# Optimization experiments

Hardware: AMD Instinct MI355X
Metric: run time of the kernel (lower is better)

The kernel has to match this reference:

```python
import jax, jax.numpy as jnp
import numpy as np

N = 50_000        # nodes
E = 1_600_000     # edges (avg degree 32)
H = 64            # hidden_channels
DEPTH = 3         # -> 2*DEPTH mid conv layers


def setup_inputs() -> dict:
    key = jax.random.key(0)
    ks = jax.random.split(key, 8)
    x = jax.random.normal(ks[0], (N, 1), dtype=jnp.float32)
    edge_index = jax.random.randint(ks[1], (2, E), 0, N, dtype=jnp.int32)
    s = 0.1  # small init scale
    W_in = s * jax.random.normal(ks[2], (2 * 1 + 1, H), dtype=jnp.float32)
    b_in = jnp.zeros((H,), jnp.float32)
    W_mid = s * jax.random.normal(ks[3], (2 * DEPTH, 2 * H + 1, H), dtype=jnp.float32)
    b_mid = jnp.zeros((2 * DEPTH, H), jnp.float32)
    W_out = s * jax.random.normal(ks[4], (2 * H + 1, 1), dtype=jnp.float32)
    b_out = jnp.zeros((1,), jnp.float32)
    return {"x": x, "edge_index": edge_index, "W_in": W_in, "b_in": b_in,
            "W_mid": W_mid, "b_mid": b_mid, "W_out": W_out, "b_out": b_out}


def _conv(x, src, dst, sign, inv_deg, W, b):
    """Directional_EdgeConv: mean_{j->i} Linear([x_i, x_j - x_i, sign(j-i)])."""
    x_i = x[dst]                                   # [E, F] target feats
    x_j = x[src]                                   # [E, F] source feats
    feat = jnp.concatenate([x_i, x_j - x_i, sign], axis=-1)  # [E, 2F+1]
    msg = feat @ W + b                             # [E, out]
    agg = jax.ops.segment_sum(msg, dst, num_segments=x.shape[0])  # [N, out]
    return agg * inv_deg                           # mean aggregation


def reference(x, edge_index, W_in, b_in, W_mid, b_mid, W_out, b_out):
    src = edge_index[0]
    dst = edge_index[1]
    # vectorized replacement of the per-edge Python sign loop
    sign = jnp.sign((src - dst).astype(x.dtype))[:, None]        # [E, 1]
    deg = jax.ops.segment_sum(jnp.ones((src.shape[0],), x.dtype), dst,
                              num_segments=x.shape[0])
    inv_deg = (1.0 / jnp.maximum(deg, 1.0))[:, None]             # [N, 1]

    x2 = _conv(x, src, dst, sign, inv_deg, W_in, b_in)
    for l in range(DEPTH):
        x1 = jax.nn.leaky_relu(
            _conv(x2, src, dst, sign, inv_deg, W_mid[2 * l], b_mid[2 * l]))
        x2 = jax.nn.leaky_relu(
            _conv(x1, src, dst, sign, inv_deg, W_mid[2 * l + 1], b_mid[2 * l + 1]) + x2)
    return _conv(x2, src, dst, sign, inv_deg, W_out, b_out) + x
```

## Files before the change

kernel.cpp:

```cpp
#include <hip/hip_runtime.h>
#include <hip/hip_fp16.h>

#define HDIM 64
#define NEG_SLOPE 0.01f
#define CAPB 8192
#define BCAP 6144

typedef _Float16 half8 __attribute__((ext_vector_type(8)));
typedef float f32x4 __attribute__((ext_vector_type(4)));

static __device__ __forceinline__ float h_lo(unsigned d) {
    return __half2float(__ushort_as_half((unsigned short)(d & 0xffffu)));
}
static __device__ __forceinline__ float h_hi(unsigned d) {
    return __half2float(__ushort_as_half((unsigned short)(d >> 16)));
}
static __device__ __forceinline__ unsigned packh(float a, float b) {
    unsigned short ra = __half_as_ushort(__float2half(a));
    unsigned short rb = __half_as_ushort(__float2half(b));
    return ((unsigned)rb << 16) | (unsigned)ra;
}
static __device__ __forceinline__ half8 u4h(uint4 v) {
    union { uint4 u; half8 h; } x; x.u = v; return x.h;
}
static __device__ __forceinline__ __half2 uh2(unsigned u) {
    union { unsigned u; __half2 h; } x; x.u = u; return x.h;
}

__global__ void k_setup(int ptotal, const float* __restrict__ W_mid,
                        unsigned short* __restrict__ WTh,
                        int NB, int* gcur, int N, unsigned* xAP, unsigned* xBP,
                        float* tvec) {
    int i = blockIdx.x * blockDim.x + threadIdx.x;
    if (i < ptotal) {
        int l = i >> 13;
        int rem = i & 8191;
        int h = rem >> 7;
        int k = rem & 127;
        const float* W = W_mid + (size_t)l * 129 * 64;
        float v = W[k * 64 + h] - ((k < 64) ? W[(64 + k) * 64 + h] : 0.f);
        WTh[i] = __half_as_ushort(__float2half(v));
    }
    if (i < NB) gcur[i] = i * CAPB;
    if (i < 32) xAP[(size_t)N * 32 + i] = 0u;
    else if (i < 64) xBP[(size_t)N * 32 + (i - 32)] = 0u;
    else if (i == 64) tvec[N] = 0.f;
}

__global__ __launch_bounds__(1024) void k_bucket(
        int E, const int* __restrict__ src, const int* __restrict__ dst,
        int* gcur, unsigned* __restrict__ bucketed, int NB) {
    __shared__ int lh[512];
    __shared__ int lbase[512];
    int t = threadIdx.x;
    int e0 = blockIdx.x * 2048;
    if (t < 512) lh[t] = 0;
    __syncthreads();
    int e1 = e0 + t, e2 = e0 + 1024 + t;
    int d1 = (e1 < E) ? dst[e1] : -1;
    int d2 = (e2 < E) ? dst[e2] : -1;
    if (d1 >= 0) atomicAdd(&lh[((unsigned)d1) >> 7], 1);
    if (d2 >= 0) atomicAdd(&lh[((unsigned)d2) >> 7], 1);
    __syncthreads();
    if (t < NB) {
        int c = lh[t];
        lbase[t] = (c > 0) ? atomicAdd(&gcur[t], c) : 0;
        lh[t] = 0;
    }
    __syncthreads();
    int s1 = (e1 < E) ? src[e1] : 0;
    int s2 = (e2 < E) ? src[e2] : 0;
    if (d1 >= 0) {
        int b = ((unsigned)d1) >> 7;
        int r = atomicAdd(&lh[b], 1);
        int pos = lbase[b] + r;
        if (pos < (b + 1) * CAPB)
            bucketed[pos] = ((unsigned)d1 << 16) | (unsigned)s1;
    }
    if (d2 >= 0) {
        int b = ((unsigned)d2) >> 7;
        int r = atomicAdd(&lh[b], 1);
        int pos = lbase[b] + r;
        if (pos < (b + 1) * CAPB)
            bucketed[pos] = ((unsigned)d2 << 16) | (unsigned)s2;
    }
}

__global__ void k_bktscan(int NB, int N, const int* __restrict__ gcur,
                          int* gstart, int* rowptr) {
    __shared__ int sd[512];
    int t = threadIdx.x;
    int c = (t < NB) ? min(gcur[t] - t * CAPB, CAPB) : 0;
    sd[t] = c;
    __syncthreads();
    int x = c;
    for (int s = 1; s < 512; s <<= 1) {
        int p = (t >= s) ? sd[t - s] : 0;
        __syncthreads();
        x += p;
        sd[t] = x;
        __syncthreads();
    }
    if (t < NB) gstart[t] = x - c;
    if (t == NB - 1) {
        gstart[NB] = x;
        rowptr[N] = x;
    }
}

__global__ void k_csr(int N, const unsigned* __restrict__ bucketed, const int* __restrict__ gcur,
                      const int* __restrict__ gstart, unsigned short* __restrict__ csr,
                      unsigned short* __restrict__ pcsr,
                      int* __restrict__ rowptr, float* __restrict__ ssinv) {
    __shared__ unsigned st[BCAP];
    __shared__ int hist[128], cur[128], excl[128], sgp[128];
    int b = blockIdx.x, t = threadIdx.x;
    int n0 = b << 7;
    int nn = min(128, N - n0);
    int cnt = min(gcur[b] - b * CAPB, CAPB);
    int base = gstart[b];
    if (t < 128) { hist[t] = 0; sgp[t] = 0; }
    unsigned sent = ((unsigned)N << 16) | (unsigned)N;
    unsigned* pb32 = (unsigned*)(pcsr + ((size_t)b << 13));
    for (int i = t; i < 4096; i += 256) pb32[i] = sent;
    __syncthreads();
    bool single = (cnt <= BCAP);
    for (int off = 0; off < cnt; off += BCAP) {
        int bs = min(BCAP, cnt - off);
        for (int i = t; i < bs; i += 256) {
            unsigned w = bucketed[b * CAPB + off + i];
            if (single) st[i] = w;
            int d = (int)(w >> 16);
            int s = (int)(w & 0xffffu);
            int dl = d - n0;
            atomicAdd(&hist[dl], 1);
            atomicAdd(&sgp[dl], ((s < d) ? 1024 : 0) + ((s == d) ? 1 : 0));
        }
    }
    __syncthreads();
    int deg_t = (t < 128) ? hist[t] : 0;
    int x = deg_t;
    for (int s = 1; s < 128; s <<= 1) {
        int p = (t < 128 && t >= s) ? hist[t - s] : 0;
        __syncthreads();
        if (t < 128) { x += p; hist[t] = x; }
        __syncthreads();
    }
    if (t < 128) {
        int ex = hist[t] - deg_t;
        excl[t] = ex;
        cur[t] = ex;
        if (t < nn) {
            rowptr[n0 + t] = base + ex;
            int sg = sgp[t];
            int lt = sg >> 10, eq = sg & 1023;
            float ss = (float)(deg_t - eq - 2 * lt);
            ssinv[n0 + t] = (deg_t > 0) ? ss / (float)deg_t : 0.f;
        }
    }
    __syncthreads();
    for (int off = 0; off < cnt; off += BCAP) {
        int bs = min(BCAP, cnt - off);
        if (!single) {
            for (int i = t; i < bs; i += 256) st[i] = bucketed[b * CAPB + off + i];
            __syncthreads();
        }
        for (int i = t; i < bs; i += 256) {
            unsigned w = st[i];
            int dl = (int)(w >> 16) - n0;
            unsigned short sval = (unsigned short)(w & 0xffffu);
            int p = atomicAdd(&cur[dl], 1);
            csr[base + p] = sval;
            int r = p - excl[dl];
            if (r < 64) pcsr[((size_t)(n0 + dl) << 6) + r] = sval;
        }
        if (!single) __syncthreads();
    }
}

__global__ void k_in(int N, const float* __restrict__ x0,
                     const int* __restrict__ rowptr, const unsigned short* __restrict__ csr,
                     const float* __restrict__ ssinv,
                     const float* __restrict__ W_in, const float* __restrict__ b_in,
                     unsigned* __restrict__ xoutP) {
    int wid = blockIdx.x * (blockDim.x >> 6) + (threadIdx.x >> 6);
    int lane = threadIdx.x & 63;
    if (wid >= N) return;
    int beg = rowptr[wid], end = rowptr[wid + 1];
    int deg = end - beg;
    float s = 0.f;
    for (int e = beg + lane; e < end; e += 64) s += x0[csr[e]];
    for (int m = 32; m >= 1; m >>= 1) s += __shfl_xor(s, m, 64);
    float invd = 1.f / (float)max(deg, 1);
    float mean = s * invd;
    float xi = x0[wid];
    float w1 = W_in[lane], w2 = W_in[64 + lane], w3 = W_in[128 + lane];
    float y = xi * (w1 - w2) + mean * w2 + ssinv[wid] * w3 + b_in[lane];
    if (deg == 0) y = 0.f;
    float ylo = __shfl(y, (2 * lane) & 63, 64);
    float yhi = __shfl(y, (2 * lane + 1) & 63, 64);
    unsigned pkd = packh(ylo, yhi);
    if (lane < 32) xoutP[(size_t)wid * 32 + lane] = pkd;
}

static __device__ __forceinline__ void chunk_acc(
        const uint4* __restrict__ xin16, int sv, int base, int sub, int lq,
        __half2& c0, __half2& c1, __half2& c2, __half2& c3) {
    int s0 = __shfl(sv, base + sub, 64);
    int s1 = __shfl(sv, base + 8 + sub, 64);
    int s2 = __shfl(sv, base + 16 + sub, 64);
    int s3 = __shfl(sv, base + 24 + sub, 64);
    uint4 d0 = xin16[(size_t)s0 * 8 + lq];
    uint4 d1 = xin16[(size_t)s1 * 8 + lq];
    uint4 d2 = xin16[(size_t)s2 * 8 + lq];
    uint4 d3 = xin16[(size_t)s3 * 8 + lq];
    c0 = __hadd2(c0, __hadd2(__hadd2(uh2(d0.x), uh2(d1.x)), __hadd2(uh2(d2.x), uh2(d3.x))));
    c1 = __hadd2(c1, __hadd2(__hadd2(uh2(d0.y), uh2(d1.y)), __hadd2(uh2(d2.y), uh2(d3.y))));
    c2 = __hadd2(c2, __hadd2(__hadd2(uh2(d0.z), uh2(d1.z)), __hadd2(uh2(d2.z), uh2(d3.z))));
    c3 = __hadd2(c3, __hadd2(__hadd2(uh2(d0.w), uh2(d1.w)), __hadd2(uh2(d2.w), uh2(d3.w))));
}

static __device__ __forceinline__ void slow_gather(
        const uint4* __restrict__ xin16, const unsigned short* __restrict__ csr,
        int beg, int end, int N, int lane, int sub, int lq, float* a) {
#pragma unroll
    for (int j = 0; j < 8; ++j) a[j] = 0.f;
    for (int tb = beg; tb < end; tb += 64) {
        int cnt = min(64, end - tb);
        int sv = (lane < cnt) ? (int)csr[tb + lane] : N;
        int ng = (cnt + 7) >> 3;
        for (int g = 0; g < ng; ++g) {
            int si = __shfl(sv, (g << 3) + sub, 64);
            uint4 d = xin16[(size_t)si * 8 + lq];
            a[0] += h_lo(d.x); a[1] += h_hi(d.x);
            a[2] += h_lo(d.y); a[3] += h_hi(d.y);
            a[4] += h_lo(d.z); a[5] += h_hi(d.z);
            a[6] += h_lo(d.w); a[7] += h_hi(d.w);
        }
    }
#pragma unroll
    for (int m = 8; m <= 32; m <<= 1) {
#pragma unroll
        for (int j = 0; j < 8; ++j) a[j] += __shfl_xor(a[j], m, 64);
    }
}

template <bool RES, bool TOUT>
__global__ __launch_bounds__(256) void k_layer(
        int N, const unsigned* __restrict__ xinP,
        const unsigned* __restrict__ xresP, unsigned* __restrict__ xoutP,
        const int* __restrict__ rowptr, const unsigned short* __restrict__ csr,
        const unsigned short* __restrict__ pcsr,
        const float* __restrict__ ssinv,
        const unsigned short* __restrict__ WThl,
        const float* __restrict__ W3, const float* __restrict__ bias,
        const float* __restrict__ Wt, float* __restrict__ tvec) {
    __shared__ unsigned Ald[16 * 64];
    __shared__ float Cld[16 * 64];
    __shared__ int sdeg[16];
    __shared__ float sss[16];

    int t = threadIdx.x;
    int lane = t & 63;
    int wv = t >> 6;
    int n0 = blockIdx.x << 4;
    int kg = lane >> 4;

    int cb = (wv << 4) + (lane & 15);
    const uint4* wp = (const uint4*)WThl;
    uint4 b0 = wp[cb * 16 + kg + 0];
    uint4 b1 = wp[cb * 16 + kg + 4];
    uint4 b2 = wp[cb * 16 + kg + 8];
    uint4 b3 = wp[cb * 16 + kg + 12];

    const uint4* xin16 = (const uint4*)xinP;
    int sub = lane >> 3;
    int lq = lane & 7;
    int ndb = wv << 2;

    int svp[4];
#pragma unroll
    for (int q = 0; q < 4; ++q)
        svp[q] = (int)pcsr[((size_t)(n0 + ndb + q) << 6) + lane];

#pragma unroll
    for (int qp = 0; qp < 2; ++qp) {
        int ndA = ndb + (qp << 1);
        int ndB = ndA + 1;
        int nodeA = n0 + ndA, nodeB = n0 + ndB;
        int ncA = min(nodeA, N - 1), ncB = min(nodeB, N - 1);
        int begA = __builtin_amdgcn_readfirstlane(rowptr[ncA]);
        int endA = __builtin_amdgcn_readfirstlane(rowptr[ncA + 1]);
        int begB = __builtin_amdgcn_readfirstlane(rowptr[ncB]);
        int endB = __builtin_amdgcn_readfirstlane(rowptr[ncB + 1]);
        int degA = (nodeA < N) ? (endA - begA) : 0;
        int degB = (nodeB < N) ? (endB - begB) : 0;
        float ssvA = ssinv[ncA];
        float ssvB = ssinv[ncB];
        uint4 xiA = make_uint4(0u, 0u, 0u, 0u), xiB = make_uint4(0u, 0u, 0u, 0u);
        if (lane < 8) {
            if (nodeA < N) xiA = xin16[(size_t)ncA * 8 + lane];
            if (nodeB < N) xiB = xin16[(size_t)ncB * 8 + lane];
        }
        uint4 mvA, mvB;
        if (max(degA, degB) <= 64) {
            __half2 z = uh2(0u);
            __half2 cA0 = z, cA1 = z, cA2 = z, cA3 = z;
            __half2 cB0 = z, cB1 = z, cB2 = z, cB3 = z;
            int svA = svp[qp << 1], svB = svp[(qp << 1) + 1];
            chunk_acc(xin16, svA, 0, sub, lq, cA0, cA1, cA2, cA3);
            chunk_acc(xin16, svB, 0, sub, lq, cB0, cB1, cB2, cB3);
            if (degA > 32) chunk_acc(xin16, svA, 32, sub, lq, cA0, cA1, cA2, cA3);
            if (degB > 32) chunk_acc(xin16, svB, 32, sub, lq, cB0, cB1, cB2, cB3);
#pragma unroll
            for (int m = 8; m <= 32; m <<= 1) {
                cA0 = __hadd2(cA0, uh2((unsigned)__shfl_xor((int)*(unsigned*)&cA0, m, 64)));
                cA1 = __hadd2(cA1, uh2((unsigned)__shfl_xor((int)*(unsigned*)&cA1, m, 64)));
                cA2 = __hadd2(cA2, uh2((unsigned)__shfl_xor((int)*(unsigned*)&cA2, m, 64)));
                cA3 = __hadd2(cA3, uh2((unsigned)__shfl_xor((int)*(unsigned*)&cA3, m, 64)));
                cB0 = __hadd2(cB0, uh2((unsigned)__shfl_xor((int)*(unsigned*)&cB0, m, 64)));
                cB1 = __hadd2(cB1, uh2((unsigned)__shfl_xor((int)*(unsigned*)&cB1, m, 64)));
                cB2 = __hadd2(cB2, uh2((unsigned)__shfl_xor((int)*(unsigned*)&cB2, m, 64)));
                cB3 = __hadd2(cB3, uh2((unsigned)__shfl_xor((int)*(unsigned*)&cB3, m, 64)));
            }
            float idA = 1.f / (float)max(degA, 1);
            float idB = 1.f / (float)max(degB, 1);
            mvA.x = packh(__half2float(__low2half(cA0)) * idA, __half2float(__high2half(cA0)) * idA);
            mvA.y = packh(__half2float(__low2half(cA1)) * idA, __half2float(__high2half(cA1)) * idA);
            mvA.z = packh(__half2float(__low2half(cA2)) * idA, __half2float(__high2half(cA2)) * idA);
            mvA.w = packh(__half2float(__low2half(cA3)) * idA, __half2float(__high2half(cA3)) * idA);
            mvB.x = packh(__half2float(__low2half(cB0)) * idB, __half2float(__high2half(cB0)) * idB);
            mvB.y = packh(__half2float(__low2half(cB1)) * idB, __half2float(__high2half(cB1)) * idB);
            mvB.z = packh(__half2float(__low2half(cB2)) * idB, __half2float(__high2half(cB2)) * idB);
            mvB.w = packh(__half2float(__low2half(cB3)) * idB, __half2float(__high2half(cB3)) * idB);
        } else {
            float aA[8], aB[8];
            slow_gather(xin16, csr, begA, endA, N, lane, sub, lq, aA);
            slow_gather(xin16, csr, begB, endB, N, lane, sub, lq, aB);
            float idA = 1.f / (float)max(degA, 1);
            float idB = 1.f / (float)max(degB, 1);
            mvA.x = packh(aA[0] * idA, aA[1] * idA);
            mvA.y = packh(aA[2] * idA, aA[3] * idA);
            mvA.z = packh(aA[4] * idA, aA[5] * idA);
            mvA.w = packh(aA[6] * idA, aA[7] * idA);
            mvB.x = packh(aB[0] * idB, aB[1] * idB);
            mvB.y = packh(aB[2] * idB, aB[3] * idB);
            mvB.z = packh(aB[4] * idB, aB[5] * idB);
            mvB.w = packh(aB[6] * idB, aB[7] * idB);
        }
        if (lane < 8) {
            int gxA = lane ^ (ndA & 7), gmA = (8 + lane) ^ (ndA & 7);
            int gxB = lane ^ (ndB & 7), gmB = (8 + lane) ^ (ndB & 7);
            ((uint4*)Ald)[ndA * 16 + gxA] = xiA;
            ((uint4*)Ald)[ndA * 16 + gmA] = mvA;
            ((uint4*)Ald)[ndB * 16 + gxB] = xiB;
            ((uint4*)Ald)[ndB * 16 + gmB] = mvB;
        }
        if (lane == 0) {
            sdeg[ndA] = degA; sss[ndA] = ssvA;
            sdeg[ndB] = degB; sss[ndB] = ssvB;
        }
    }
    __syncthreads();

    int r = lane & 15;
    const uint4* ap = (const uint4*)Ald;
    int rx = (r & 7);
    uint4 fa0 = ap[r * 16 + ((0 + kg) ^ rx)];
    uint4 fa1 = ap[r * 16 + ((4 + kg) ^ rx)];
    uint4 fa2 = ap[r * 16 + ((8 + kg) ^ rx)];
    uint4 fa3 = ap[r * 16 + ((12 + kg) ^ rx)];
    f32x4 acc = {0.f, 0.f, 0.f, 0.f};
    acc = __builtin_amdgcn_mfma_f32_16x16x32_f16(u4h(fa0), u4h(b0), acc, 0, 0, 0);
    acc = __builtin_amdgcn_mfma_f32_16x16x32_f16(u4h(fa1), u4h(b1), acc, 0, 0, 0);
    acc = __builtin_amdgcn_mfma_f32_16x16x32_f16(u4h(fa2), u4h(b2), acc, 0, 0, 0);
    acc = __builtin_amdgcn_mfma_f32_16x16x32_f16(u4h(fa3), u4h(b3), acc, 0, 0, 0);
#pragma unroll
    for (int reg = 0; reg < 4; ++reg)
        Cld[(kg * 4 + reg) * 64 + (wv << 4) + r] = acc[reg];
    __syncthreads();

    int nd = t >> 4;
    int node = n0 + nd;
    if (node < N) {
        int dg = sdeg[nd];
        float ss = sss[nd];
        float tp = 0.f;
#pragma unroll
        for (int jj = 0; jj < 2; ++jj) {
            int j = (t & 15) + jj * 16;
            float y0 = Cld[nd * 64 + 2 * j];
            float y1 = Cld[nd * 64 + 2 * j + 1];
            float2 w3 = ((const float2*)W3)[j];
            float2 bb = ((const float2*)bias)[j];
            y0 += ss * w3.x + bb.x;
            y1 += ss * w3.y + bb.y;
            if (dg == 0) { y0 = 0.f; y1 = 0.f; }
            if (RES) {
                unsigned rw = xresP[(size_t)node * 32 + j];
                y0 += h_lo(rw);
                y1 += h_hi(rw);
            }
            y0 = (y0 > 0.f) ? y0 : NEG_SLOPE * y0;
            y1 = (y1 > 0.f) ? y1 : NEG_SLOPE * y1;
            if (TOUT) {
                float2 wt = ((const float2*)Wt)[j];
                tp += y0 * wt.x + y1 * wt.y;
            }
            xoutP[(size_t)node * 32 + j] = packh(y0, y1);
        }
        if (TOUT) {
            tp += __shfl_xor(tp, 1, 64);
            tp += __shfl_xor(tp, 2, 64);
            tp += __shfl_xor(tp, 4, 64);
            tp += __shfl_xor(tp, 8, 64);
            if ((t & 15) == 0) tvec[node] = tp;
        }
    }
}

__global__ void k_out(int N, const unsigned* __restrict__ xAP, const float* __restrict__ x0,
                      const int* __restrict__ rowptr, const unsigned short* __restrict__ csr,
                      const unsigned short* __restrict__ pcsr,
                      const float* __restrict__ ssinv, const float* __restrict__ t,
                      const float* __restrict__ W_out, const float* __restrict__ b_out,
                      float* __restrict__ out) {
    int wid = blockIdx.x * (blockDim.x >> 6) + (threadIdx.x >> 6);
    int lane = threadIdx.x & 63;
    if (wid >= N) return;
    int beg = rowptr[wid], end = rowptr[wid + 1];
    int deg = end - beg;
    float s;
    if (deg <= 64) {
        int sl = (int)pcsr[((size_t)wid << 6) + lane];
        s = t[sl];
    } else {
        s = 0.f;
        for (int e = beg + lane; e < end; e += 64) s += t[csr[e]];
    }
    unsigned xw = xAP[(size_t)wid * 32 + (lane >> 1)];
    float xf = (lane & 1) ? h_hi(xw) : h_lo(xw);
    float p = xf * (W_out[lane] - W_out[64 + lane]);
    for (int m = 32; m >= 1; m >>= 1) {
        s += __shfl_xor(s, m, 64);
        p += __shfl_xor(p, m, 64);
    }
    float invd = 1.f / (float)max(deg, 1);
    float y = p + s * invd + ssinv[wid] * W_out[128] + b_out[0];
    if (deg == 0) y = 0.f;
    if (lane == 0) out[wid] = y + x0[wid];
}

static inline size_t align16(size_t x) { return (x + 15) & ~(size_t)15; }

extern "C" void kernel_launch(void* const* d_in, const int* in_sizes, int n_in,
                              void* d_out, int out_size, void* d_ws, size_t ws_size,
                              hipStream_t stream) {
    const float* x0    = (const float*)d_in[0];
    const int*   ei    = (const int*)d_in[1];
    const float* W_in  = (const float*)d_in[2];
    const float* b_in  = (const float*)d_in[3];
    const float* W_mid = (const float*)d_in[4];
    const float* b_mid = (const float*)d_in[5];
    const float* W_out = (const float*)d_in[6];
    const float* b_out = (const float*)d_in[7];
    float* out = (float*)d_out;

    const int N = in_sizes[0];
    const int E = in_sizes[1] / 2;
    const int L = in_sizes[4] / (129 * 64);
    const int NB = (N + 127) >> 7;
    const int* src = ei;
    const int* dst = ei + E;

    char* p = (char*)d_ws;
    unsigned short* WTh = (unsigned short*)p; p += align16((size_t)L * 64 * 128 * 2);
    unsigned* xAP = (unsigned*)p; p += align16((size_t)(N + 1) * 32 * 4);
    unsigned* xBP = (unsigned*)p; p += align16((size_t)(N + 1) * 32 * 4);
    unsigned* bucketed = (unsigned*)p; p += align16((size_t)NB * CAPB * 4);
    unsigned short* csr = (unsigned short*)p; p += align16((size_t)E * 2);
    unsigned short* pcsr = (unsigned short*)p; p += align16((size_t)NB * 8192 * 2);
    int* gcur          = (int*)p; p += align16((size_t)(NB + 1) * 4);
    int* gstart        = (int*)p; p += align16((size_t)(NB + 1) * 4);
    int* rowptr        = (int*)p; p += align16((size_t)(N + 1) * 4);
    float* ssinv       = (float*)p; p += align16((size_t)N * 4);
    float* t           = (float*)p; p += align16((size_t)(N + 1) * 4);

    const int nb_w4 = (N + 3) / 4;
    const int nb_bkt = (E + 2047) / 2048;
    const int ptotal = L * 64 * 128;
    const int nb_lay = (N + 15) / 16;

    k_setup<<<(ptotal + 255) / 256, 256, 0, stream>>>(ptotal, W_mid, WTh, NB, gcur, N, xAP, xBP, t);
    k_bucket<<<nb_bkt, 1024, 0, stream>>>(E, src, dst, gcur, bucketed, NB);
    k_bktscan<<<1, 512, 0, stream>>>(NB, N, gcur, gstart, rowptr);
    k_csr<<<NB, 256, 0, stream>>>(N, bucketed, gcur, gstart, csr, pcsr, rowptr, ssinv);

    k_in<<<nb_w4, 256, 0, stream>>>(N, x0, rowptr, csr, ssinv, W_in, b_in, xAP);

    for (int l = 0; l < L / 2; ++l) {
        bool last = (l == L / 2 - 1);
        const unsigned short* Wa = WTh + (size_t)(2 * l) * 64 * 128;
        const unsigned short* Wb = WTh + (size_t)(2 * l + 1) * 64 * 128;
        const float* W3a = W_mid + (size_t)(2 * l) * 129 * 64 + 128 * 64;
        const float* W3b = W_mid + (size_t)(2 * l + 1) * 129 * 64 + 128 * 64;

        k_layer<false, false><<<nb_lay, 256, 0, stream>>>(
            N, xAP, nullptr, xBP, rowptr, csr, pcsr, ssinv,
            Wa, W3a, b_mid + (size_t)(2 * l) * HDIM, nullptr, nullptr);
        if (!last) {
            k_layer<true, false><<<nb_lay, 256, 0, stream>>>(
                N, xBP, xAP, xAP, rowptr, csr, pcsr, ssinv,
                Wb, W3b, b_mid + (size_t)(2 * l + 1) * HDIM, nullptr, nullptr);
        } else {
            k_layer<true, true><<<nb_lay, 256, 0, stream>>>(
                N, xBP, xAP, xAP, rowptr, csr, pcsr, ssinv,
                Wb, W3b, b_mid + (size_t)(2 * l + 1) * HDIM, W_out + 64, t);
        }
    }

    k_out<<<nb_w4, 256, 0, stream>>>(N, xAP, x0, rowptr, csr, pcsr, ssinv, t,
                                     W_out, b_out, out);
}
```

Measured before the change: 253.8 us.

## Double waves per layer block, split MFMA K across wave halves

The layer kernel now launches 512 threads per 16-node block instead of 256. Each wave gathers neighbours for 2 nodes instead of 4, and the 128-wide K dimension of the MFMA GEMM is split across two wave groups. The two partial results go to separate LDS buffers and are summed in the epilogue, with one thread per output pair. The aim is more concurrent gather traffic and shorter per-wave latency chains, at the cost of a larger block, extra LDS, and an extra add per output.

```diff
diff --git a/kernel.cpp b/kernel.cpp
--- a/kernel.cpp
+++ b/kernel.cpp
@@ -246,7 +246,7 @@
 }
 
 template <bool RES, bool TOUT>
-__global__ __launch_bounds__(256) void k_layer(
+__global__ __launch_bounds__(512) void k_layer(
         int N, const unsigned* __restrict__ xinP,
         const unsigned* __restrict__ xresP, unsigned* __restrict__ xoutP,
         const int* __restrict__ rowptr, const unsigned short* __restrict__ csr,
@@ -256,7 +256,7 @@
         const float* __restrict__ W3, const float* __restrict__ bias,
         const float* __restrict__ Wt, float* __restrict__ tvec) {
     __shared__ unsigned Ald[16 * 64];
-    __shared__ float Cld[16 * 64];
+    __shared__ float Cld[2][16 * 64];
     __shared__ int sdeg[16];
     __shared__ float sss[16];
 
@@ -265,156 +265,139 @@
     int wv = t >> 6;
     int n0 = blockIdx.x << 4;
     int kg = lane >> 4;
-
-    int cb = (wv << 4) + (lane & 15);
+    int htile = wv & 3;
+    int khalf = wv >> 2;
+
+    int cb = (htile << 4) + (lane & 15);
     const uint4* wp = (const uint4*)WThl;
-    uint4 b0 = wp[cb * 16 + kg + 0];
-    uint4 b1 = wp[cb * 16 + kg + 4];
-    uint4 b2 = wp[cb * 16 + kg + 8];
-    uint4 b3 = wp[cb * 16 + kg + 12];
+    uint4 b0 = wp[cb * 16 + khalf * 8 + kg];
+    uint4 b1 = wp[cb * 16 + khalf * 8 + 4 + kg];
 
     const uint4* xin16 = (const uint4*)xinP;
     int sub = lane >> 3;
     int lq = lane & 7;
-    int ndb = wv << 2;
-
-    int svp[4];
+
+    int ndA = wv << 1;
+    int ndB = ndA + 1;
+    int nodeA = n0 + ndA, nodeB = n0 + ndB;
+    int ncA = min(nodeA, N - 1), ncB = min(nodeB, N - 1);
+    int svA = (int)pcsr[((size_t)nodeA << 6) + lane];
+    int svB = (int)pcsr[((size_t)nodeB << 6) + lane];
+    int begA = __builtin_amdgcn_readfirstlane(rowptr[ncA]);
+    int endA = __builtin_amdgcn_readfirstlane(rowptr[ncA + 1]);
+    int begB = __builtin_amdgcn_readfirstlane(rowptr[ncB]);
+    int endB = __builtin_amdgcn_readfirstlane(rowptr[ncB + 1]);
+    int degA = (nodeA < N) ? (endA - begA) : 0;
+    int degB = (nodeB < N) ? (endB - begB) : 0;
+    float ssvA = ssinv[ncA];
+    float ssvB = ssinv[ncB];
+    uint4 xiA = make_uint4(0u, 0u, 0u, 0u), xiB = make_uint4(0u, 0u, 0u, 0u);
+    if (lane < 8) {
+        if (nodeA < N) xiA = xin16[(size_t)ncA * 8 + lane];
+        if (nodeB < N) xiB = xin16[(size_t)ncB * 8 + lane];
+    }
+    uint4 mvA, mvB;
+    if (max(degA, degB) <= 64) {
+        __half2 z = uh2(0u);
+        __half2 cA0 = z, cA1 = z, cA2 = z, cA3 = z;
+        __half2 cB0 = z, cB1 = z, cB2 = z, cB3 = z;
+        chunk_acc(xin16, svA, 0, sub, lq, cA0, cA1, cA2, cA3);
+        chunk_acc(xin16, svB, 0, sub, lq, cB0, cB1, cB2, cB3);
+        if (degA > 32) chunk_acc(xin16, svA, 32, sub, lq, cA0, cA1, cA2, cA3);
+        if (degB > 32) chunk_acc(xin16, svB, 32, sub, lq, cB0, cB1, cB2, cB3);
 #pragma unroll
-    for (int q = 0; q < 4; ++q)
-        svp[q] = (int)pcsr[((size_t)(n0 + ndb + q) << 6) + lane];
-
-#pragma unroll
-    for (int qp = 0; qp < 2; ++qp) {
-        int ndA = ndb + (qp << 1);
-        int ndB = ndA + 1;
-        int nodeA = n0 + ndA, nodeB = n0 + ndB;
-        int ncA = min(nodeA, N - 1), ncB = min(nodeB, N - 1);
-        int begA = __builtin_amdgcn_readfirstlane(rowptr[ncA]);
-        int endA = __builtin_amdgcn_readfirstlane(rowptr[ncA + 1]);
-        int begB = __builtin_amdgcn_readfirstlane(rowptr[ncB]);
-        int endB = __builtin_amdgcn_readfirstlane(rowptr[ncB + 1]);
-        int degA = (nodeA < N) ? (endA - begA) : 0;
-        int degB = (nodeB < N) ? (endB - begB) : 0;
-        float ssvA = ssinv[ncA];
-        float ssvB = ssinv[ncB];
-        uint4 xiA = make_uint4(0u, 0u, 0u, 0u), xiB = make_uint4(0u, 0u, 0u, 0u);
-        if (lane < 8) {
-            if (nodeA < N) xiA = xin16[(size_t)ncA * 8 + lane];
-            if (nodeB < N) xiB = xin16[(size_t)ncB * 8 + lane];
-        }
-        uint4 mvA, mvB;
-        if (max(degA, degB) <= 64) {
-            __half2 z = uh2(0u);
-            __half2 cA0 = z, cA1 = z, cA2 = z, cA3 = z;
-            __half2 cB0 = z, cB1 = z, cB2 = z, cB3 = z;
-            int svA = svp[qp << 1], svB = svp[(qp << 1) + 1];
-            chunk_acc(xin16, svA, 0, sub, lq, cA0, cA1, cA2, cA3);
-            chunk_acc(xin16, svB, 0, sub, lq, cB0, cB1, cB2, cB3);
-            if (degA > 32) chunk_acc(xin16, svA, 32, sub, lq, cA0, cA1, cA2, cA3);
-            if (degB > 32) chunk_acc(xin16, svB, 32, sub, lq, cB0, cB1, cB2, cB3);
-#pragma unroll
-            for (int m = 8; m <= 32; m <<= 1) {
-                cA0 = __hadd2(cA0, uh2((unsigned)__shfl_xor((int)*(unsigned*)&cA0, m, 64)));
-                cA1 = __hadd2(cA1, uh2((unsigned)__shfl_xor((int)*(unsigned*)&cA1, m, 64)));
-                cA2 = __hadd2(cA2, uh2((unsigned)__shfl_xor((int)*(unsigned*)&cA2, m, 64)));
-                cA3 = __hadd2(cA3, uh2((unsigned)__shfl_xor((int)*(unsigned*)&cA3, m, 64)));
-                cB0 = __hadd2(cB0, uh2((unsigned)__shfl_xor((int)*(unsigned*)&cB0, m, 64)));
-                cB1 = __hadd2(cB1, uh2((unsigned)__shfl_xor((int)*(unsigned*)&cB1, m, 64)));
-                cB2 = __hadd2(cB2, uh2((unsigned)__shfl_xor((int)*(unsigned*)&cB2, m, 64)));
-                cB3 = __hadd2(cB3, uh2((unsigned)__shfl_xor((int)*(unsigned*)&cB3, m, 64)));
-            }
-            float idA = 1.f / (float)max(degA, 1);
-            float idB = 1.f / (float)max(degB, 1);
-            mvA.x = packh(__half2float(__low2half(cA0)) * idA, __half2float(__high2half(cA0)) * idA);
-            mvA.y = packh(__half2float(__low2half(cA1)) * idA, __half2float(__high2half(cA1)) * idA);
-            mvA.z = packh(__half2float(__low2half(cA2)) * idA, __half2float(__high2half(cA2)) * idA);
-            mvA.w = packh(__half2float(__low2half(cA3)) * idA, __half2float(__high2half(cA3)) * idA);
-            mvB.x = packh(__half2float(__low2half(cB0)) * idB, __half2float(__high2half(cB0)) * idB);
-            mvB.y = packh(__half2float(__low2half(cB1)) * idB, __half2float(__high2half(cB1)) * idB);
-            mvB.z = packh(__half2float(__low2half(cB2)) * idB, __half2float(__high2half(cB2)) * idB);
-            mvB.w = packh(__half2float(__low2half(cB3)) * idB, __half2float(__high2half(cB3)) * idB);
-        } else {
-            float aA[8], aB[8];
-            slow_gather(xin16, csr, begA, endA, N, lane, sub, lq, aA);
-            slow_gather(xin16, csr, begB, endB, N, lane, sub, lq, aB);
-            float idA = 1.f / (float)max(degA, 1);
-            float idB = 1.f / (float)max(degB, 1);
-            mvA.x = packh(aA[0] * idA, aA[1] * idA);
-            mvA.y = packh(aA[2] * idA, aA[3] * idA);
-            mvA.z = packh(aA[4] * idA, aA[5] * idA);
-            mvA.w = packh(aA[6] * idA, aA[7] * idA);
-            mvB.x = packh(aB[0] * idB, aB[1] * idB);
-            mvB.y = packh(aB[2] * idB, aB[3] * idB);
-            mvB.z = packh(aB[4] * idB, aB[5] * idB);
-            mvB.w = packh(aB[6] * idB, aB[7] * idB);
-        }
-        if (lane < 8) {
-            int gxA = lane ^ (ndA & 7), gmA = (8 + lane) ^ (ndA & 7);
-            int gxB = lane ^ (ndB & 7), gmB = (8 + lane) ^ (ndB & 7);
-            ((uint4*)Ald)[ndA * 16 + gxA] = xiA;
-            ((uint4*)Ald)[ndA * 16 + gmA] = mvA;
-            ((uint4*)Ald)[ndB * 16 + gxB] = xiB;
-            ((uint4*)Ald)[ndB * 16 + gmB] = mvB;
-        }
-        if (lane == 0) {
-            sdeg[ndA] = degA; sss[ndA] = ssvA;
-            sdeg[ndB] = degB; sss[ndB] = ssvB;
-        }
+        for (int m = 8; m <= 32; m <<= 1) {
+            cA0 = __hadd2(cA0, uh2((unsigned)__shfl_xor((int)*(unsigned*)&cA0, m, 64)));
+            cA1 = __hadd2(cA1, uh2((unsigned)__shfl_xor((int)*(unsigned*)&cA1, m, 64)));
+            cA2 = __hadd2(cA2, uh2((unsigned)__shfl_xor((int)*(unsigned*)&cA2, m, 64)));
+            cA3 = __hadd2(cA3, uh2((unsigned)__shfl_xor((int)*(unsigned*)&cA3, m, 64)));
+            cB0 = __hadd2(cB0, uh2((unsigned)__shfl_xor((int)*(unsigned*)&cB0, m, 64)));
+            cB1 = __hadd2(cB1, uh2((unsigned)__shfl_xor((int)*(unsigned*)&cB1, m, 64)));
+            cB2 = __hadd2(cB2, uh2((unsigned)__shfl_xor((int)*(unsigned*)&cB2, m, 64)));
+            cB3 = __hadd2(cB3, uh2((unsigned)__shfl_xor((int)*(unsigned*)&cB3, m, 64)));
+        }
+        float idA = 1.f / (float)max(degA, 1);
+        float idB = 1.f / (float)max(degB, 1);
+        mvA.x = packh(__half2float(__low2half(cA0)) * idA, __half2float(__high2half(cA0)) * idA);
+        mvA.y = packh(__half2float(__low2half(cA1)) * idA, __half2float(__high2half(cA1)) * idA);
+        mvA.z = packh(__half2float(__low2half(cA2)) * idA, __half2float(__high2half(cA2)) * idA);
+        mvA.w = packh(__half2float(__low2half(cA3)) * idA, __half2float(__high2half(cA3)) * idA);
+        mvB.x = packh(__half2float(__low2half(cB0)) * idB, __half2float(__high2half(cB0)) * idB);
+        mvB.y = packh(__half2float(__low2half(cB1)) * idB, __half2float(__high2half(cB1)) * idB);
+        mvB.z = packh(__half2float(__low2half(cB2)) * idB, __half2float(__high2half(cB2)) * idB);
+        mvB.w = packh(__half2float(__low2half(cB3)) * idB, __half2float(__high2half(cB3)) * idB);
+    } else {
+        float aA[8], aB[8];
+        slow_gather(xin16, csr, begA, endA, N, lane, sub, lq, aA);
+        slow_gather(xin16, csr, begB, endB, N, lane, sub, lq, aB);
+        float idA = 1.f / (float)max(degA, 1);
+        float idB = 1.f / (float)max(degB, 1);
+        mvA.x = packh(aA[0] * idA, aA[1] * idA);
+        mvA.y = packh(aA[2] * idA, aA[3] * idA);
+        mvA.z = packh(aA[4] * idA, aA[5] * idA);
+        mvA.w = packh(aA[6] * idA, aA[7] * idA);
+        mvB.x = packh(aB[0] * idB, aB[1] * idB);
+        mvB.y = packh(aB[2] * idB, aB[3] * idB);
+        mvB.z = packh(aB[4] * idB, aB[5] * idB);
+        mvB.w = packh(aB[6] * idB, aB[7] * idB);
+    }
+    if (lane < 8) {
+        int gxA = lane ^ (ndA & 7), gmA = (8 + lane) ^ (ndA & 7);
+        int gxB = lane ^ (ndB & 7), gmB = (8 + lane) ^ (ndB & 7);
+        ((uint4*)Ald)[ndA * 16 + gxA] = xiA;
+        ((uint4*)Ald)[ndA * 16 + gmA] = mvA;
+        ((uint4*)Ald)[ndB * 16 + gxB] = xiB;
+        ((uint4*)Ald)[ndB * 16 + gmB] = mvB;
+    }
+    if (lane == 0) {
+        sdeg[ndA] = degA; sss[ndA] = ssvA;
+        sdeg[ndB] = degB; sss[ndB] = ssvB;
     }
     __syncthreads();
 
     int r = lane & 15;
     const uint4* ap = (const uint4*)Ald;
     int rx = (r & 7);
-    uint4 fa0 = ap[r * 16 + ((0 + kg) ^ rx)];
-    uint4 fa1 = ap[r * 16 + ((4 + kg) ^ rx)];
-    uint4 fa2 = ap[r * 16 + ((8 + kg) ^ rx)];
-    uint4 fa3 = ap[r * 16 + ((12 + kg) ^ rx)];
+    uint4 fa0 = ap[r * 16 + ((khalf * 8 + kg) ^ rx)];
+    uint4 fa1 = ap[r * 16 + ((khalf * 8 + 4 + kg) ^ rx)];
     f32x4 acc = {0.f, 0.f, 0.f, 0.f};
     acc = __builtin_amdgcn_mfma_f32_16x16x32_f16(u4h(fa0), u4h(b0), acc, 0, 0, 0);
     acc = __builtin_amdgcn_mfma_f32_16x16x32_f16(u4h(fa1), u4h(b1), acc, 0, 0, 0);
-    acc = __builtin_amdgcn_mfma_f32_16x16x32_f16(u4h(fa2), u4h(b2), acc, 0, 0, 0);
-    acc = __builtin_amdgcn_mfma_f32_16x16x32_f16(u4h(fa3), u4h(b3), acc, 0, 0, 0);
 #pragma unroll
     for (int reg = 0; reg < 4; ++reg)
-        Cld[(kg * 4 + reg) * 64 + (wv << 4) + r] = acc[reg];
-    __syncthreads();
-
-    int nd = t >> 4;
+        Cld[khalf][(kg * 4 + reg) * 64 + (htile << 4) + r] = acc[reg];
+    __syncthreads();
+
+    int nd = t >> 5;
     int node = n0 + nd;
     if (node < N) {
         int dg = sdeg[nd];
         float ss = sss[nd];
-        float tp = 0.f;
-#pragma unroll
-        for (int jj = 0; jj < 2; ++jj) {
-            int j = (t & 15) + jj * 16;
-            float y0 = Cld[nd * 64 + 2 * j];
-            float y1 = Cld[nd * 64 + 2 * j + 1];
-            float2 w3 = ((const float2*)W3)[j];
-            float2 bb = ((const float2*)bias)[j];
-            y0 += ss * w3.x + bb.x;
-            y1 += ss * w3.y + bb.y;
-            if (dg == 0) { y0 = 0.f; y1 = 0.f; }
-            if (RES) {
-                unsigned rw = xresP[(size_t)node * 32 + j];
-                y0 += h_lo(rw);
-                y1 += h_hi(rw);
-            }
-            y0 = (y0 > 0.f) ? y0 : NEG_SLOPE * y0;
-            y1 = (y1 > 0.f) ? y1 : NEG_SLOPE * y1;
-            if (TOUT) {
-                float2 wt = ((const float2*)Wt)[j];
-                tp += y0 * wt.x + y1 * wt.y;
-            }
-            xoutP[(size_t)node * 32 + j] = packh(y0, y1);
-        }
+        int j = t & 31;
+        float y0 = Cld[0][nd * 64 + 2 * j] + Cld[1][nd * 64 + 2 * j];
+        float y1 = Cld[0][nd * 64 + 2 * j + 1] + Cld[1][nd * 64 + 2 * j + 1];
+        float2 w3 = ((const float2*)W3)[j];
+        float2 bb = ((const float2*)bias)[j];
+        y0 += ss * w3.x + bb.x;
+        y1 += ss * w3.y + bb.y;
+        if (dg == 0) { y0 = 0.f; y1 = 0.f; }
+        if (RES) {
+            unsigned rw = xresP[(size_t)node * 32 + j];
+            y0 += h_lo(rw);
+            y1 += h_hi(rw);
+        }
+        y0 = (y0 > 0.f) ? y0 : NEG_SLOPE * y0;
+        y1 = (y1 > 0.f) ? y1 : NEG_SLOPE * y1;
+        xoutP[(size_t)node * 32 + j] = packh(y0, y1);
         if (TOUT) {
+            float2 wt = ((const float2*)Wt)[j];
+            float tp = y0 * wt.x + y1 * wt.y;
             tp += __shfl_xor(tp, 1, 64);
             tp += __shfl_xor(tp, 2, 64);
             tp += __shfl_xor(tp, 4, 64);
             tp += __shfl_xor(tp, 8, 64);
-            if ((t & 15) == 0) tvec[node] = tp;
+            tp += __shfl_xor(tp, 16, 64);
+            if (j == 0) tvec[node] = tp;
         }
     }
 }
@@ -505,15 +488,15 @@
         const float* W3a = W_mid + (size_t)(2 * l) * 129 * 64 + 128 * 64;
         const float* W3b = W_mid + (size_t)(2 * l + 1) * 129 * 64 + 128 * 64;
 
-        k_layer<false, false><<<nb_lay, 256, 0, stream>>>(
+        k_layer<false, false><<<nb_lay, 512, 0, stream>>>(
             N, xAP, nullptr, xBP, rowptr, csr, pcsr, ssinv,
             Wa, W3a, b_mid + (size_t)(2 * l) * HDIM, nullptr, nullptr);
         if (!last) {
-            k_layer<true, false><<<nb_lay, 256, 0, stream>>>(
+            k_layer<true, false><<<nb_lay, 512, 0, stream>>>(
                 N, xBP, xAP, xAP, rowptr, csr, pcsr, ssinv,
                 Wb, W3b, b_mid + (size_t)(2 * l + 1) * HDIM, nullptr, nullptr);
         } else {
-            k_layer<true, true><<<nb_lay, 256, 0, stream>>>(
+            k_layer<true, true><<<nb_lay, 512, 0, stream>>>(
                 N, xBP, xAP, xAP, rowptr, csr, pcsr, ssinv,
                 Wb, W3b, b_mid + (size_t)(2 * l + 1) * HDIM, W_out + 64, t);
         }
```

Result: slower. 258.9 us (+2.0%).

## Locally sort edges in bucket kernel and fold bucket scan into CSR kernel

Applied to the files above, without the earlier changes.

The bucketing kernel now handles 4096 edges per block and sorts them by bucket in shared memory before writing, so global stores to each bucket become contiguous runs instead of scattered writes. The separate single-block bucket-scan kernel is removed, and each CSR block recomputes the prefix over bucket counts itself, which drops one launch and its serialization. The CSR kernel moves to 512 threads. In exchange every CSR block repeats a 512-entry scan, and the bucket kernel uses more shared memory and barriers.

```diff
diff --git a/kernel.cpp b/kernel.cpp
--- a/kernel.cpp
+++ b/kernel.cpp
@@ -5,6 +5,7 @@
 #define NEG_SLOPE 0.01f
 #define CAPB 8192
 #define BCAP 6144
+#define EPB  4096
 
 typedef _Float16 half8 __attribute__((ext_vector_type(8)));
 typedef float f32x4 __attribute__((ext_vector_type(4)));
@@ -51,83 +52,87 @@
         int E, const int* __restrict__ src, const int* __restrict__ dst,
         int* gcur, unsigned* __restrict__ bucketed, int NB) {
     __shared__ int lh[512];
+    __shared__ int sd[512];
     __shared__ int lbase[512];
+    __shared__ unsigned sorted[EPB];
     int t = threadIdx.x;
-    int e0 = blockIdx.x * 2048;
+    int e0 = blockIdx.x * EPB;
     if (t < 512) lh[t] = 0;
     __syncthreads();
-    int e1 = e0 + t, e2 = e0 + 1024 + t;
-    int d1 = (e1 < E) ? dst[e1] : -1;
-    int d2 = (e2 < E) ? dst[e2] : -1;
-    if (d1 >= 0) atomicAdd(&lh[((unsigned)d1) >> 7], 1);
-    if (d2 >= 0) atomicAdd(&lh[((unsigned)d2) >> 7], 1);
-    __syncthreads();
-    if (t < NB) {
-        int c = lh[t];
+    int dv[4], sv[4], rv[4];
+#pragma unroll
+    for (int k = 0; k < 4; ++k) {
+        int e = e0 + k * 1024 + t;
+        dv[k] = (e < E) ? dst[e] : -1;
+        sv[k] = (e < E) ? src[e] : 0;
+    }
+#pragma unroll
+    for (int k = 0; k < 4; ++k)
+        rv[k] = (dv[k] >= 0) ? atomicAdd(&lh[((unsigned)dv[k]) >> 7], 1) : 0;
+    __syncthreads();
+    int c = (t < 512) ? lh[t] : 0;
+    if (t < 512) {
         lbase[t] = (c > 0) ? atomicAdd(&gcur[t], c) : 0;
-        lh[t] = 0;
-    }
-    __syncthreads();
-    int s1 = (e1 < E) ? src[e1] : 0;
-    int s2 = (e2 < E) ? src[e2] : 0;
-    if (d1 >= 0) {
-        int b = ((unsigned)d1) >> 7;
-        int r = atomicAdd(&lh[b], 1);
-        int pos = lbase[b] + r;
-        if (pos < (b + 1) * CAPB)
-            bucketed[pos] = ((unsigned)d1 << 16) | (unsigned)s1;
-    }
-    if (d2 >= 0) {
-        int b = ((unsigned)d2) >> 7;
-        int r = atomicAdd(&lh[b], 1);
-        int pos = lbase[b] + r;
-        if (pos < (b + 1) * CAPB)
-            bucketed[pos] = ((unsigned)d2 << 16) | (unsigned)s2;
-    }
-}
-
-__global__ void k_bktscan(int NB, int N, const int* __restrict__ gcur,
-                          int* gstart, int* rowptr) {
-    __shared__ int sd[512];
-    int t = threadIdx.x;
-    int c = (t < NB) ? min(gcur[t] - t * CAPB, CAPB) : 0;
-    sd[t] = c;
+        sd[t] = c;
+    }
     __syncthreads();
     int x = c;
     for (int s = 1; s < 512; s <<= 1) {
-        int p = (t >= s) ? sd[t - s] : 0;
+        int p = (t < 512 && t >= s) ? sd[t - s] : 0;
         __syncthreads();
-        x += p;
-        sd[t] = x;
+        if (t < 512) { x += p; sd[t] = x; }
         __syncthreads();
     }
-    if (t < NB) gstart[t] = x - c;
-    if (t == NB - 1) {
-        gstart[NB] = x;
-        rowptr[N] = x;
-    }
-}
-
-__global__ void k_csr(int N, const unsigned* __restrict__ bucketed, const int* __restrict__ gcur,
-                      const int* __restrict__ gstart, unsigned short* __restrict__ csr,
-                      unsigned short* __restrict__ pcsr,
-                      int* __restrict__ rowptr, float* __restrict__ ssinv) {
+#pragma unroll
+    for (int k = 0; k < 4; ++k) {
+        if (dv[k] >= 0) {
+            int b = ((unsigned)dv[k]) >> 7;
+            sorted[sd[b] - lh[b] + rv[k]] = ((unsigned)dv[k] << 16) | (unsigned)sv[k];
+        }
+    }
+    __syncthreads();
+    int ntot = sd[511];
+    for (int i = t; i < ntot; i += 1024) {
+        unsigned w = sorted[i];
+        int b = (int)(w >> 23);
+        int pos = lbase[b] + (i - (sd[b] - lh[b]));
+        if (pos < (b + 1) * CAPB) bucketed[pos] = w;
+    }
+}
+
+__global__ __launch_bounds__(512) void k_csr(
+        int N, int NB, const unsigned* __restrict__ bucketed, const int* __restrict__ gcur,
+        unsigned short* __restrict__ csr, unsigned short* __restrict__ pcsr,
+        int* __restrict__ rowptr, float* __restrict__ ssinv) {
     __shared__ unsigned st[BCAP];
     __shared__ int hist[128], cur[128], excl[128], sgp[128];
+    __shared__ int gsd[512];
     int b = blockIdx.x, t = threadIdx.x;
     int n0 = b << 7;
     int nn = min(128, N - n0);
+    int cc = (t < NB) ? min(gcur[t] - t * CAPB, CAPB) : 0;
+    gsd[t] = cc;
+    __syncthreads();
+    int xs = cc;
+    for (int s = 1; s < 512; s <<= 1) {
+        int p = (t >= s) ? gsd[t - s] : 0;
+        __syncthreads();
+        xs += p;
+        gsd[t] = xs;
+        __syncthreads();
+    }
     int cnt = min(gcur[b] - b * CAPB, CAPB);
-    int base = gstart[b];
+    int base = gsd[b] - cnt;
+    if (b == NB - 1 && t == 0) rowptr[N] = gsd[NB - 1];
     if (t < 128) { hist[t] = 0; sgp[t] = 0; }
     unsigned sent = ((unsigned)N << 16) | (unsigned)N;
     unsigned* pb32 = (unsigned*)(pcsr + ((size_t)b << 13));
-    for (int i = t; i < 4096; i += 256) pb32[i] = sent;
+    for (int i = t; i < 4096; i += 512) pb32[i] = sent;
     __syncthreads();
     bool single = (cnt <= BCAP);
     for (int off = 0; off < cnt; off += BCAP) {
         int bs = min(BCAP, cnt - off);
-        for (int i = t; i < bs; i += 256) {
+        for (int i = t; i < bs; i += 512) {
             unsigned w = bucketed[b * CAPB + off + i];
             if (single) st[i] = w;
             int d = (int)(w >> 16);
@@ -162,10 +167,10 @@
     for (int off = 0; off < cnt; off += BCAP) {
         int bs = min(BCAP, cnt - off);
         if (!single) {
-            for (int i = t; i < bs; i += 256) st[i] = bucketed[b * CAPB + off + i];
+            for (int i = t; i < bs; i += 512) st[i] = bucketed[b * CAPB + off + i];
             __syncthreads();
         }
-        for (int i = t; i < bs; i += 256) {
+        for (int i = t; i < bs; i += 512) {
             unsigned w = st[i];
             int dl = (int)(w >> 16) - n0;
             unsigned short sval = (unsigned short)(w & 0xffffu);
@@ -481,20 +486,18 @@
     unsigned short* csr = (unsigned short*)p; p += align16((size_t)E * 2);
     unsigned short* pcsr = (unsigned short*)p; p += align16((size_t)NB * 8192 * 2);
     int* gcur          = (int*)p; p += align16((size_t)(NB + 1) * 4);
-    int* gstart        = (int*)p; p += align16((size_t)(NB + 1) * 4);
     int* rowptr        = (int*)p; p += align16((size_t)(N + 1) * 4);
     float* ssinv       = (float*)p; p += align16((size_t)N * 4);
     float* t           = (float*)p; p += align16((size_t)(N + 1) * 4);
 
     const int nb_w4 = (N + 3) / 4;
-    const int nb_bkt = (E + 2047) / 2048;
+    const int nb_bkt = (E + EPB - 1) / EPB;
     const int ptotal = L * 64 * 128;
     const int nb_lay = (N + 15) / 16;
 
     k_setup<<<(ptotal + 255) / 256, 256, 0, stream>>>(ptotal, W_mid, WTh, NB, gcur, N, xAP, xBP, t);
     k_bucket<<<nb_bkt, 1024, 0, stream>>>(E, src, dst, gcur, bucketed, NB);
-    k_bktscan<<<1, 512, 0, stream>>>(NB, N, gcur, gstart, rowptr);
-    k_csr<<<NB, 256, 0, stream>>>(N, bucketed, gcur, gstart, csr, pcsr, rowptr, ssinv);
+    k_csr<<<NB, 512, 0, stream>>>(N, NB, bucketed, gcur, csr, pcsr, rowptr, ssinv);
 
     k_in<<<nb_w4, 256, 0, stream>>>(N, x0, rowptr, csr, ssinv, W_in, b_in, xAP);
 
```

New measurement: 242.5 us. -4.5%, faster.
